# Optimization experiments

Measured on AMD Instinct MI355X. Metric: run time of the kernel, lower is better.

## Reference

```python
import jax, jax.numpy as jnp
import numpy as np
from jax import lax


def _batch_conv(x, w, b):
    # x: [B, Cin, H, W], w: [B, Cout, Cin, kh, kw], b: [B, Cout]
    # Per-sample conv (the torch code's groups=B grouped-conv trick),
    # expressed as vmap over the batch of an ordinary conv.
    def one(xi, wi):
        return lax.conv_general_dilated(
            xi[None], wi, window_strides=(1, 1), padding='SAME',
            dimension_numbers=('NCHW', 'OIHW', 'NCHW'))[0]
    y = jax.vmap(one)(x, w)                       # [B, Cout, H, W]
    return y + b[:, :, None, None]


def setup_inputs() -> dict:
    key = jax.random.key(0)
    ks = jax.random.split(key, 9)
    B, Cin, H, W = 32, 3, 64, 64
    NC = 10
    s = 0.05
    return {
        'x': jax.random.normal(ks[0], (B, Cin, H, W), jnp.float32),
        'conv1_weight': jax.random.normal(ks[1], (B, 64, Cin, 3, 3), jnp.float32) * s,
        'conv2_weight': jax.random.normal(ks[2], (B, 128, 64, 3, 3), jnp.float32) * s,
        'conv3_weight': jax.random.normal(ks[3], (B, 256, 128, 3, 3), jnp.float32) * s,
        'fc_weight': jax.random.normal(ks[4], (B, 1, NC), jnp.float32) * s,
        'bias1': jax.random.normal(ks[5], (B, 64), jnp.float32) * s,
        'bias2': jax.random.normal(ks[6], (B, 128), jnp.float32) * s,
        'bias3': jax.random.normal(ks[7], (B, 256), jnp.float32) * s,
        'bias4': jax.random.normal(ks[8], (B, NC), jnp.float32) * s,
    }


def reference(x, conv1_weight, conv2_weight, conv3_weight, fc_weight,
              bias1, bias2, bias3, bias4):
    h = jax.nn.relu(_batch_conv(x, conv1_weight, bias1))   # [B, 64, H, W]
    h = jax.nn.relu(_batch_conv(h, conv2_weight, bias2))   # [B, 128, H, W]
    h = jax.nn.relu(_batch_conv(h, conv3_weight, bias3))   # [B, 256, H, W]
    h = jnp.mean(h, axis=(2, 3))                           # AdaptiveAvgPool2d(1) -> [B, 256]
    h = h[:, :, None]                                      # view(B, N, -1) -> [B, 256, 1]
    # BatchLinearLayer: bmm(x, weight) + bias
    out = jnp.einsum('bnd,bdo->bno', h, fc_weight) + bias4[:, None, :]  # [B, 256, 10]
    return out
```

## Files before the change

kernel.cpp:

```cpp
#include <hip/hip_runtime.h>
#include <stdint.h>

typedef __attribute__((ext_vector_type(8))) short short8;
typedef __attribute__((ext_vector_type(16))) float f32x16;

#define NB 32

__device__ __forceinline__ float bf2f(uint16_t v) {
    return __uint_as_float(((uint32_t)v) << 16);
}
__device__ __forceinline__ uint16_t f2bf(float f) {
    uint32_t u = __float_as_uint(f);
    u += 0x7fffu + ((u >> 16) & 1u);
    return (uint16_t)(u >> 16);
}

__device__ __forceinline__ void gload16(const void* g, void* l) {
    __builtin_amdgcn_global_load_lds(
        (const __attribute__((address_space(1))) uint32_t*)g,
        (__attribute__((address_space(3))) uint32_t*)l, 16, 0, 0);
}

template<int COUT, int CIN>
__device__ __forceinline__ void prep_w_item(int idx, const float* __restrict__ w,
                                            uint16_t* __restrict__ wp)
{
    const int ci = idx % CIN;
    const int t  = idx / CIN;
    const int oc = t % COUT;
    const int b  = t / COUT;
    const float* s = w + (size_t)idx * 9;
    #pragma unroll
    for (int k = 0; k < 9; k++)
        wp[((size_t)(b * 9 + k) * COUT + oc) * CIN + ci] = f2bf(s[k]);
}

__global__ __launch_bounds__(256) void prep_w3_k(
    const float* __restrict__ w, uint16_t* __restrict__ wp)
{
    const int idx = blockIdx.x * 256 + threadIdx.x;
    if (idx < NB * 256 * 128) prep_w_item<256, 128>(idx, w, wp);
}

template<bool DO_W3>
__global__ __launch_bounds__(256) void prep_all(
    const float* __restrict__ x,  const float* __restrict__ w1,
    const float* __restrict__ w2, const float* __restrict__ w3,
    uint16_t* __restrict__ xp,  uint16_t* __restrict__ wp1,
    uint16_t* __restrict__ wp2, uint16_t* __restrict__ wp3,
    float* __restrict__ zp)
{
    int idx = blockIdx.x * 256 + threadIdx.x;
    if (idx < 4096) {
        ((float4*)zp)[idx] = make_float4(0.f, 0.f, 0.f, 0.f);
        return;
    }
    idx -= 4096;
    if (idx < 131072) {
        const int xc = idx & 63, y = (idx >> 6) & 63, b = idx >> 12;
        const float* s = x + (size_t)b * 3 * 4096 + y * 64 + xc;
        const uint16_t v0 = f2bf(s[0]), v1 = f2bf(s[4096]), v2 = f2bf(s[8192]);
        short8 lo = {(short)v0, (short)v1, (short)v2, 0, 0, 0, 0, 0};
        short8 hi = {0, 0, 0, 0, 0, 0, 0, 0};
        uint16_t* d = xp + (size_t)idx * 16;
        *(short8*)d = lo;
        *(short8*)(d + 8) = hi;
        return;
    }
    idx -= 131072;
    if (idx < 18432) {
        const int oc = idx & 63, k = (idx >> 6) % 9, b = idx / 576;
        const uint16_t v0 = f2bf(w1[((size_t)(b * 64 + oc) * 3 + 0) * 9 + k]);
        const uint16_t v1 = f2bf(w1[((size_t)(b * 64 + oc) * 3 + 1) * 9 + k]);
        const uint16_t v2 = f2bf(w1[((size_t)(b * 64 + oc) * 3 + 2) * 9 + k]);
        short8 lo = {(short)v0, (short)v1, (short)v2, 0, 0, 0, 0, 0};
        short8 hi = {0, 0, 0, 0, 0, 0, 0, 0};
        uint16_t* d = wp1 + ((size_t)(b * 9 + k) * 64 + oc) * 16;
        *(short8*)d = lo;
        *(short8*)(d + 8) = hi;
        return;
    }
    idx -= 18432;
    if (idx < 262144) {
        prep_w_item<128, 64>(idx, w2, wp2);
        return;
    }
    if (!DO_W3) return;
    idx -= 262144;
    if (idx < 1048576) prep_w_item<256, 128>(idx, w3, wp3);
}

template<int CIN, int COUT, int OCBLKS, bool POOL>
__global__ __launch_bounds__(256, 2) void conv_mfma(
    const uint16_t* __restrict__ in, const uint16_t* __restrict__ wp,
    const float* __restrict__ bias, uint16_t* __restrict__ out,
    float* __restrict__ partial, const float* __restrict__ zp)
{
    constexpr int IN_CH = 21;
    constexpr int W_CH  = 18;
    constexpr int IN_B  = IN_CH * 1024;
    constexpr int BUF_B = IN_B + W_CH * 1024;
    constexpr int P     = OCBLKS * 8;
    extern __shared__ __align__(16) char sm[];

    const int L   = blockIdx.x;
    const int xcd = L & 7;
    const int jj  = L >> 3;
    const int b   = (jj / P) * 8 + xcd;
    const int inner = jj % P;
    const int ocbase = (inner >> 3) * 64;
    const int stripe = inner & 7;
    const int y0 = stripe * 8;

    const int tid = threadIdx.x;
    const int wv = tid >> 6, l = tid & 63, q = l >> 5, ln = l & 31;
    const int NK = CIN / 16;

    const uint16_t* srcp[10];
    int ldsoff[10];
    #pragma unroll
    for (int j = 0; j < 10; j++) {
        const int chunk = wv * 10 + j;
        if (chunk >= IN_CH + W_CH) {
            srcp[j] = (const uint16_t*)zp;
            ldsoff[j] = -1;
        } else if (chunk < IN_CH) {
            const int gp = chunk * 64 + l;
            const int g = gp ^ ((gp >> 3) & 7);
            const int qq = g & 1, site = g >> 1;
            const int row = site / 66, px = site - row * 66;
            const int gy = y0 - 1 + row, gx = px - 1;
            const bool valid = (row < 10) && ((unsigned)gy < 64u) && ((unsigned)gx < 64u);
            srcp[j] = valid ? in + ((size_t)((b * 64 + gy) * 64 + gx) * CIN + qq * 8)
                            : (const uint16_t*)zp;
            ldsoff[j] = chunk * 1024;
        } else {
            const int gp = (chunk - IN_CH) * 64 + l;
            const int g = gp ^ ((gp >> 3) & 7);
            const int qq = g & 1, kk = g >> 7, oc = (g >> 1) & 63;
            srcp[j] = wp + ((size_t)(b * 9 + kk) * COUT + ocbase + oc) * CIN + qq * 8;
            ldsoff[j] = IN_B + (chunk - IN_CH) * 1024;
        }
    }

    int aoff[4][3][2];
    #pragma unroll
    for (int t = 0; t < 4; t++)
        #pragma unroll
        for (int kx = 0; kx < 3; kx++)
            #pragma unroll
            for (int h = 0; h < 2; h++) {
                const int g = ((wv * 2 + t) * 66 + h * 32 + ln + kx) * 2 + q;
                aoff[t][kx][h] = (g ^ ((g >> 3) & 7)) * 16;
            }
    const int gb = ln * 2 + q;
    const int boff = (gb ^ ((gb >> 3) & 7)) * 16;

    f32x16 aA0, aA1, aB0, aB1, aC0, aC1, aD0, aD1;
    {
        const float bv0 = bias[b * COUT + ocbase + ln];
        const float bv1 = bias[b * COUT + ocbase + 32 + ln];
        #pragma unroll
        for (int r = 0; r < 16; r++) {
            aA0[r] = bv0; aB0[r] = bv0; aC0[r] = bv0; aD0[r] = bv0;
            aA1[r] = bv1; aB1[r] = bv1; aC1[r] = bv1; aD1[r] = bv1;
        }
    }

    auto stage = [&](int bufsel, int k) {
        const int koff = k * 16;
        char* base = sm + bufsel * BUF_B;
        #pragma unroll
        for (int j = 0; j < 10; j++) {
            char* dst = (ldsoff[j] < 0) ? (sm + 2 * BUF_B)
                                        : (base + ldsoff[j]);
            gload16(srcp[j] + koff, dst);
        }
    };

    stage(0, 0);
    if (NK > 1) stage(1, 1);

    for (int k = 0; k < NK; k++) {
        const char* cb = sm + (k & 1) * BUF_B;
        if (k + 1 < NK) asm volatile("s_waitcnt vmcnt(10)" ::: "memory");
        else            asm volatile("s_waitcnt vmcnt(0)"  ::: "memory");
        __builtin_amdgcn_s_barrier();
        __builtin_amdgcn_sched_barrier(0);
        __builtin_amdgcn_s_setprio(1);
        #pragma unroll
        for (int ky = 0; ky < 3; ky++)
            #pragma unroll
            for (int kx = 0; kx < 3; kx++) {
                const int kk = ky * 3 + kx;
                short8 fA = *(const short8*)(cb + aoff[ky + 0][kx][0]);
                short8 fB = *(const short8*)(cb + aoff[ky + 0][kx][1]);
                short8 fC = *(const short8*)(cb + aoff[ky + 1][kx][0]);
                short8 fD = *(const short8*)(cb + aoff[ky + 1][kx][1]);
                const char* bw = cb + IN_B + kk * 2048 + boff;
                short8 b0 = *(const short8*)(bw);
                short8 b1 = *(const short8*)(bw + 1024);
                aA0 = __builtin_amdgcn_mfma_f32_32x32x16_bf16(fA, b0, aA0, 0, 0, 0);
                aB0 = __builtin_amdgcn_mfma_f32_32x32x16_bf16(fB, b0, aB0, 0, 0, 0);
                aC0 = __builtin_amdgcn_mfma_f32_32x32x16_bf16(fC, b0, aC0, 0, 0, 0);
                aD0 = __builtin_amdgcn_mfma_f32_32x32x16_bf16(fD, b0, aD0, 0, 0, 0);
                aA1 = __builtin_amdgcn_mfma_f32_32x32x16_bf16(fA, b1, aA1, 0, 0, 0);
                aB1 = __builtin_amdgcn_mfma_f32_32x32x16_bf16(fB, b1, aB1, 0, 0, 0);
                aC1 = __builtin_amdgcn_mfma_f32_32x32x16_bf16(fC, b1, aC1, 0, 0, 0);
                aD1 = __builtin_amdgcn_mfma_f32_32x32x16_bf16(fD, b1, aD1, 0, 0, 0);
            }
        __builtin_amdgcn_s_setprio(0);
        __builtin_amdgcn_s_barrier();
        if (k + 2 < NK) stage(k & 1, k + 2);
    }

    if (!POOL) {
        #pragma unroll
        for (int r = 0; r < 16; r++) {
            const int pxr = (r & 3) + 8 * (r >> 2) + 4 * q;
            const int y0w = y0 + wv * 2;
            uint16_t* dA = out + (size_t)((b * 64 + y0w) * 64 + pxr) * COUT + ocbase;
            uint16_t* dB = out + (size_t)((b * 64 + y0w) * 64 + 32 + pxr) * COUT + ocbase;
            uint16_t* dC = out + (size_t)((b * 64 + y0w + 1) * 64 + pxr) * COUT + ocbase;
            uint16_t* dD = out + (size_t)((b * 64 + y0w + 1) * 64 + 32 + pxr) * COUT + ocbase;
            dA[ln]      = f2bf(fmaxf(aA0[r], 0.f));
            dA[32 + ln] = f2bf(fmaxf(aA1[r], 0.f));
            dB[ln]      = f2bf(fmaxf(aB0[r], 0.f));
            dB[32 + ln] = f2bf(fmaxf(aB1[r], 0.f));
            dC[ln]      = f2bf(fmaxf(aC0[r], 0.f));
            dC[32 + ln] = f2bf(fmaxf(aC1[r], 0.f));
            dD[ln]      = f2bf(fmaxf(aD0[r], 0.f));
            dD[32 + ln] = f2bf(fmaxf(aD1[r], 0.f));
        }
    } else {
        float* red = (float*)(sm + 2 * BUF_B + 1024);
        float s0 = 0.f, s1 = 0.f;
        #pragma unroll
        for (int r = 0; r < 16; r++) {
            s0 += fmaxf(aA0[r], 0.f) + fmaxf(aB0[r], 0.f)
                + fmaxf(aC0[r], 0.f) + fmaxf(aD0[r], 0.f);
            s1 += fmaxf(aA1[r], 0.f) + fmaxf(aB1[r], 0.f)
                + fmaxf(aC1[r], 0.f) + fmaxf(aD1[r], 0.f);
        }
        s0 += __shfl_xor(s0, 32);
        s1 += __shfl_xor(s1, 32);
        if (q == 0) {
            red[wv * 64 + ln] = s0;
            red[wv * 64 + 32 + ln] = s1;
        }
        __syncthreads();
        if (tid < 64) {
            float t = red[tid] + red[64 + tid] + red[128 + tid] + red[192 + tid];
            partial[(size_t)(b * 256 + ocbase + tid) * 8 + stripe] = t;
        }
    }
}

__global__ void fc_k(const float* __restrict__ partial,
                     const float* __restrict__ fcw,
                     const float* __restrict__ b4, float* __restrict__ out)
{
    const int b = blockIdx.x, c = threadIdx.x;
    const float* p = partial + (size_t)(b * 256 + c) * 8;
    float s = 0.f;
    #pragma unroll
    for (int i = 0; i < 8; i++) s += p[i];
    const float pooled = s * (1.f / 4096.f);
    #pragma unroll
    for (int o = 0; o < 10; o++)
        out[(b * 256 + c) * 10 + o] = fmaf(pooled, fcw[b * 10 + o], b4[b * 10 + o]);
}

extern "C" void kernel_launch(void* const* d_in, const int* in_sizes, int n_in,
                              void* d_out, int out_size, void* d_ws, size_t ws_size,
                              hipStream_t stream)
{
    const float* x   = (const float*)d_in[0];
    const float* w1  = (const float*)d_in[1];
    const float* w2  = (const float*)d_in[2];
    const float* w3  = (const float*)d_in[3];
    const float* fcw = (const float*)d_in[4];
    const float* b1  = (const float*)d_in[5];
    const float* b2  = (const float*)d_in[6];
    const float* b3  = (const float*)d_in[7];
    const float* b4  = (const float*)d_in[8];
    char* ws = (char*)d_ws;
    uint16_t* xp  = (uint16_t*)(ws);
    uint16_t* wp1 = (uint16_t*)(ws + 4194304);
    uint16_t* h2  = (uint16_t*)(ws);
    uint16_t* h1  = (uint16_t*)(ws + 33554432);
    uint16_t* wp2 = (uint16_t*)(ws + 50331648);
    const bool big_ws = ws_size >= 74186752u;
    uint16_t* wp3     = (uint16_t*)(ws + (big_ws ? 55050240u : 33554432u));
    float*    partial = (float*)   (ws + (big_ws ? 73924608u : 52428800u));
    float*    zp      = (float*)d_out;

    constexpr int DYN_LDS = 2 * 39936 + 1024 + 1024;
    static bool attr_done = false;
    if (!attr_done) {
        hipFuncSetAttribute((const void*)&conv_mfma<16, 64, 1, false>,
                            hipFuncAttributeMaxDynamicSharedMemorySize, DYN_LDS);
        hipFuncSetAttribute((const void*)&conv_mfma<64, 128, 2, false>,
                            hipFuncAttributeMaxDynamicSharedMemorySize, DYN_LDS);
        hipFuncSetAttribute((const void*)&conv_mfma<128, 256, 4, true>,
                            hipFuncAttributeMaxDynamicSharedMemorySize, DYN_LDS);
        attr_done = true;
    }

    if (big_ws) {
        prep_all<true><<<5720, 256, 0, stream>>>(x, w1, w2, w3, xp, wp1, wp2, wp3, zp);
    } else {
        prep_all<false><<<1624, 256, 0, stream>>>(x, w1, w2, w3, xp, wp1, wp2, wp3, zp);
    }
    conv_mfma<16, 64, 1, false><<<NB * 8, 256, DYN_LDS, stream>>>(xp, wp1, b1, h1, nullptr, zp);
    conv_mfma<64, 128, 2, false><<<NB * 16, 256, DYN_LDS, stream>>>(h1, wp2, b2, h2, nullptr, zp);
    if (!big_ws)
        prep_w3_k<<<4096, 256, 0, stream>>>(w3, wp3);
    conv_mfma<128, 256, 4, true><<<NB * 32, 256, DYN_LDS, stream>>>(h2, wp3, b3, nullptr, partial, zp);
    fc_k<<<NB, 256, 0, stream>>>(partial, fcw, b4, (float*)d_out);
}
```

Baseline: 122.4 us.

## Drop LDS swizzle, use plane-major input layout and reuse A fragments across ky

The input tile in LDS moves from an XOR-swizzled interleaved layout to a plain [row][k-half][pixel] layout. Weights move to a [tap][k-half][oc] layout, so each lane's 16-byte read is contiguous. The inner loop is reordered to kx-outer. The eight A fragments for the four rows are loaded once per kx and reused across the three ky taps, which cuts LDS reads per K-step from 54 to 42. The cost is about 32 more live VGPRs for the fragment cache, and bank conflicts may change now that the swizzle is gone.

```diff
diff --git a/kernel.cpp b/kernel.cpp
--- a/kernel.cpp
+++ b/kernel.cpp
@@ -126,35 +126,28 @@
             ldsoff[j] = -1;
         } else if (chunk < IN_CH) {
             const int gp = chunk * 64 + l;
-            const int g = gp ^ ((gp >> 3) & 7);
-            const int qq = g & 1, site = g >> 1;
-            const int row = site / 66, px = site - row * 66;
+            const int rq = gp / 66, px = gp - rq * 66;
+            const int row = rq >> 1, qq = rq & 1;
             const int gy = y0 - 1 + row, gx = px - 1;
-            const bool valid = (row < 10) && ((unsigned)gy < 64u) && ((unsigned)gx < 64u);
+            const bool valid = (rq < 20) && ((unsigned)gy < 64u) && ((unsigned)gx < 64u);
             srcp[j] = valid ? in + ((size_t)((b * 64 + gy) * 64 + gx) * CIN + qq * 8)
                             : (const uint16_t*)zp;
             ldsoff[j] = chunk * 1024;
         } else {
-            const int gp = (chunk - IN_CH) * 64 + l;
-            const int g = gp ^ ((gp >> 3) & 7);
-            const int qq = g & 1, kk = g >> 7, oc = (g >> 1) & 63;
+            const int c2 = chunk - IN_CH;
+            const int kk = c2 >> 1, qq = c2 & 1, oc = l;
             srcp[j] = wp + ((size_t)(b * 9 + kk) * COUT + ocbase + oc) * CIN + qq * 8;
-            ldsoff[j] = IN_B + (chunk - IN_CH) * 1024;
-        }
-    }
-
-    int aoff[4][3][2];
+            ldsoff[j] = IN_B + c2 * 1024;
+        }
+    }
+
+    int aoffA[4][2];
     #pragma unroll
     for (int t = 0; t < 4; t++)
         #pragma unroll
-        for (int kx = 0; kx < 3; kx++)
-            #pragma unroll
-            for (int h = 0; h < 2; h++) {
-                const int g = ((wv * 2 + t) * 66 + h * 32 + ln + kx) * 2 + q;
-                aoff[t][kx][h] = (g ^ ((g >> 3) & 7)) * 16;
-            }
-    const int gb = ln * 2 + q;
-    const int boff = (gb ^ ((gb >> 3) & 7)) * 16;
+        for (int h = 0; h < 2; h++)
+            aoffA[t][h] = ((((wv * 2 + t) * 2 + q) * 66) + h * 32 + ln) * 16;
+    const int boffB = q * 1024 + ln * 16;
 
     f32x16 aA0, aA1, aB0, aB1, aC0, aC1, aD0, aD1;
     {
@@ -189,26 +182,29 @@
         __builtin_amdgcn_sched_barrier(0);
         __builtin_amdgcn_s_setprio(1);
         #pragma unroll
-        for (int ky = 0; ky < 3; ky++)
+        for (int kx = 0; kx < 3; kx++) {
+            short8 fA[4][2];
             #pragma unroll
-            for (int kx = 0; kx < 3; kx++) {
+            for (int t = 0; t < 4; t++)
+                #pragma unroll
+                for (int h = 0; h < 2; h++)
+                    fA[t][h] = *(const short8*)(cb + aoffA[t][h] + kx * 16);
+            #pragma unroll
+            for (int ky = 0; ky < 3; ky++) {
                 const int kk = ky * 3 + kx;
-                short8 fA = *(const short8*)(cb + aoff[ky + 0][kx][0]);
-                short8 fB = *(const short8*)(cb + aoff[ky + 0][kx][1]);
-                short8 fC = *(const short8*)(cb + aoff[ky + 1][kx][0]);
-                short8 fD = *(const short8*)(cb + aoff[ky + 1][kx][1]);
-                const char* bw = cb + IN_B + kk * 2048 + boff;
+                const char* bw = cb + IN_B + kk * 2048 + boffB;
                 short8 b0 = *(const short8*)(bw);
-                short8 b1 = *(const short8*)(bw + 1024);
-                aA0 = __builtin_amdgcn_mfma_f32_32x32x16_bf16(fA, b0, aA0, 0, 0, 0);
-                aB0 = __builtin_amdgcn_mfma_f32_32x32x16_bf16(fB, b0, aB0, 0, 0, 0);
-                aC0 = __builtin_amdgcn_mfma_f32_32x32x16_bf16(fC, b0, aC0, 0, 0, 0);
-                aD0 = __builtin_amdgcn_mfma_f32_32x32x16_bf16(fD, b0, aD0, 0, 0, 0);
-                aA1 = __builtin_amdgcn_mfma_f32_32x32x16_bf16(fA, b1, aA1, 0, 0, 0);
-                aB1 = __builtin_amdgcn_mfma_f32_32x32x16_bf16(fB, b1, aB1, 0, 0, 0);
-                aC1 = __builtin_amdgcn_mfma_f32_32x32x16_bf16(fC, b1, aC1, 0, 0, 0);
-                aD1 = __builtin_amdgcn_mfma_f32_32x32x16_bf16(fD, b1, aD1, 0, 0, 0);
+                short8 b1 = *(const short8*)(bw + 512);
+                aA0 = __builtin_amdgcn_mfma_f32_32x32x16_bf16(fA[ky][0], b0, aA0, 0, 0, 0);
+                aB0 = __builtin_amdgcn_mfma_f32_32x32x16_bf16(fA[ky][1], b0, aB0, 0, 0, 0);
+                aC0 = __builtin_amdgcn_mfma_f32_32x32x16_bf16(fA[ky + 1][0], b0, aC0, 0, 0, 0);
+                aD0 = __builtin_amdgcn_mfma_f32_32x32x16_bf16(fA[ky + 1][1], b0, aD0, 0, 0, 0);
+                aA1 = __builtin_amdgcn_mfma_f32_32x32x16_bf16(fA[ky][0], b1, aA1, 0, 0, 0);
+                aB1 = __builtin_amdgcn_mfma_f32_32x32x16_bf16(fA[ky][1], b1, aB1, 0, 0, 0);
+                aC1 = __builtin_amdgcn_mfma_f32_32x32x16_bf16(fA[ky + 1][0], b1, aC1, 0, 0, 0);
+                aD1 = __builtin_amdgcn_mfma_f32_32x32x16_bf16(fA[ky + 1][1], b1, aD1, 0, 0, 0);
             }
+        }
         __builtin_amdgcn_s_setprio(0);
         __builtin_amdgcn_s_barrier();
         if (k + 2 < NK) stage(k & 1, k + 2);
```

New measurement: 132.9 us. +8.6%, slower.
